# Performance work log

Measured on AMD Instinct MI355X. Metric: run time of the kernel, lower is better.

## Reference

```python
import jax, jax.numpy as jnp
import numpy as np

N = 4096      # nnode
F = 128       # feature_dim
E = 64        # embed_dim
P_EDGE = 0.01 # edge probability (~41 avg degree)
NEG = -9e15
ALPHA = 0.2   # leaky relu slope


def _xavier(key, shape):
    lim = float(np.sqrt(6.0 / (shape[0] + shape[1])))
    return jax.random.uniform(key, shape, minval=-lim, maxval=lim, dtype=jnp.float32)


def setup_inputs() -> dict:
    key = jax.random.key(0)
    ks = jax.random.split(key, 14)
    features = jax.random.normal(ks[0], (N, F), dtype=jnp.float32)
    eye = jnp.eye(N, dtype=jnp.float32)

    def make_adj(k):
        a = (jax.random.uniform(k, (N, N)) < P_EDGE).astype(jnp.float32)
        return jnp.maximum(a, eye)  # self loop so no empty rows

    return {
        "features": features,
        "geo_adj": make_adj(ks[1]),
        "forward_adj": make_adj(ks[2]),
        "backward_adj": make_adj(ks[3]),
        "weight": _xavier(ks[4], (E, F)),
        "Wf": _xavier(ks[5], (F, E)),
        "af1": jax.random.normal(ks[6], (E,), dtype=jnp.float32) * 0.1,
        "af2": jax.random.normal(ks[7], (E,), dtype=jnp.float32) * 0.1,
        "Wb": _xavier(ks[8], (F, E)),
        "ab1": jax.random.normal(ks[9], (E,), dtype=jnp.float32) * 0.1,
        "ab2": jax.random.normal(ks[10], (E,), dtype=jnp.float32) * 0.1,
        "Wg": _xavier(ks[11], (F, E)),
        "ag1": jax.random.normal(ks[12], (E,), dtype=jnp.float32) * 0.1,
        "ag2": jax.random.normal(ks[13], (E,), dtype=jnp.float32) * 0.1,
    }


def _mean_neighbors(adj, feat):
    # pre_weight: row-normalized neighbor averaging, (N,N) @ (N,F)
    deg = jnp.clip(jnp.sum(adj, axis=1, keepdims=True), 1.0, None)
    return (adj @ feat) / deg


def _attention(feat, mask_feat, adj, W, a1, a2):
    # GAT-style additive attention with masked softmax over neighbors
    h = feat @ W        # (N, E)
    hm = mask_feat @ W  # (N, E)
    e = jax.nn.leaky_relu((h @ a1)[:, None] + (hm @ a2)[None, :], negative_slope=ALPHA)  # (N, N)
    e = jnp.where(adj > 0, e, NEG)
    return jax.nn.softmax(e, axis=1)  # (N, N)


def reference(features, geo_adj, forward_adj, backward_adj, weight,
              Wf, af1, af2, Wb, ab1, ab2, Wg, ag1, ag2):
    t = features  # (N, F)
    mask_f = _mean_neighbors(forward_adj, t)
    mask_b = _mean_neighbors(backward_adj, t)
    mask_g = _mean_neighbors(geo_adj, t)

    w_f = _attention(t, mask_f, forward_adj, Wf, af1, af2)
    w_b = _attention(t, mask_b, backward_adj, Wb, ab1, ab2)
    w_g = _attention(t, mask_g, geo_adj, Wg, ag1, ag2)

    # get_mask_matrix_i/_j broadcast-mul + sum(1) == attn @ t (or attn.T @ t)
    x = weight @ t.T                  # (E, N)
    x_fwd = weight @ (w_f @ t).T      # mask_matrix_i
    x_bwd = weight @ (w_b.T @ t).T    # mask_matrix_j (transposed)
    x_geo = weight @ (w_g @ t).T      # mask_matrix_i

    return jnp.concatenate([x, x_fwd, x_bwd, x_geo], axis=0)  # (4E, N)
```

## Files before the change

### kernel.cpp

```cpp
#include <hip/hip_runtime.h>

#define NN 4096
#define FF 128
#define EE 64

typedef unsigned short u16;
typedef unsigned long long u64;
typedef float vf4 __attribute__((ext_vector_type(4)));

__device__ __forceinline__ float lrelu(float x) { return x > 0.f ? x : 0.2f * x; }

__global__ __launch_bounds__(256)
void k_pre(const float* __restrict__ t, const float* __restrict__ weight,
           const float* __restrict__ Wf, const float* __restrict__ af1, const float* __restrict__ af2,
           const float* __restrict__ Wb, const float* __restrict__ ab1, const float* __restrict__ ab2,
           const float* __restrict__ Wg, const float* __restrict__ ag1, const float* __restrict__ ag2,
           float* __restrict__ u, float* __restrict__ s1, float* __restrict__ p,
           float* __restrict__ out, int* __restrict__ ccnt)
{
    __shared__ float ww[64 * 129];
    __shared__ float tt[16 * 130];
    __shared__ float uacc[64 * 17];
    __shared__ float w6[6 * FF];
    int b = blockIdx.x, tid = threadIdx.x;

    if (b < 64) {
        if (b < 16) ccnt[b * 256 + tid] = 0;
        const float* Ws[3]  = {Wf, Wb, Wg};
        const float* a1s[3] = {af1, ab1, ag1};
        const float* a2s[3] = {af2, ab2, ag2};
        for (int idx = tid; idx < 768; idx += 256) {
            int vi = idx >> 7, f = idx & 127, dd = vi >> 1;
            const float4* a4 = reinterpret_cast<const float4*>((vi & 1) ? a2s[dd] : a1s[dd]);
            const float4* W4 = reinterpret_cast<const float4*>(Ws[dd] + (size_t)f * EE);
            float s = 0.f;
            #pragma unroll
            for (int e4 = 0; e4 < 16; ++e4) {
                float4 wv = W4[e4], av = a4[e4];
                s += wv.x * av.x + wv.y * av.y + wv.z * av.z + wv.w * av.w;
            }
            w6[vi * FF + f] = s;
        }
        __syncthreads();
        int nb = b * 64;
        for (int idx = tid; idx < 384; idx += 256) {
            int n = idx & 63, vi = idx >> 6;
            const float4* t4 = reinterpret_cast<const float4*>(t + (size_t)(nb + n) * FF);
            const float* wv = &w6[vi * FF];
            float s = 0.f;
            #pragma unroll 8
            for (int q4 = 0; q4 < 32; ++q4) {
                float4 v = t4[q4];
                s += v.x * wv[q4 * 4] + v.y * wv[q4 * 4 + 1]
                   + v.z * wv[q4 * 4 + 2] + v.w * wv[q4 * 4 + 3];
            }
            int dd = vi >> 1;
            if (vi & 1) p[dd * NN + nb + n] = s; else s1[dd * NN + nb + n] = s;
        }
        return;
    }

    int n0 = (b - 64) * 16;
    const float4* w4 = reinterpret_cast<const float4*>(weight);
    for (int i = tid; i < 2048; i += 256) {
        float4 v = w4[i];
        int fi = i * 4, e = fi >> 7, q = fi & 127;
        float* dst = &ww[e * 129 + q];
        dst[0] = v.x; dst[1] = v.y; dst[2] = v.z; dst[3] = v.w;
    }
    const float4* t4 = reinterpret_cast<const float4*>(t + (size_t)n0 * FF);
    for (int i = tid; i < 512; i += 256) {
        float4 v = t4[i];
        int fi = i * 4, nd = fi >> 7, q = fi & 127;
        float* dst = &tt[nd * 130 + q];
        dst[0] = v.x; dst[1] = v.y; dst[2] = v.z; dst[3] = v.w;
    }
    __syncthreads();
    int g = tid >> 6, lane = tid & 63;
    for (int k = 0; k < 4; ++k) {
        int nd = g * 4 + k;
        const float* trow = &tt[nd * 130];
        const float* wrow = &ww[lane * 129];
        float acc = 0.f;
        #pragma unroll 16
        for (int q = 0; q < 128; ++q) acc += wrow[q] * trow[q];
        u[(size_t)(n0 + nd) * EE + lane] = acc;
        uacc[lane * 17 + nd] = acc;
    }
    __syncthreads();
    int e = tid >> 2, io = (tid & 3) * 4;
    float* orow = out + (size_t)e * NN + n0 + io;
    orow[0] = uacc[e * 17 + io];
    orow[1] = uacc[e * 17 + io + 1];
    orow[2] = uacc[e * 17 + io + 2];
    orow[3] = uacc[e * 17 + io + 3];
}

__global__ __launch_bounds__(256, 8)
void k_scan(const float* __restrict__ Af, const float* __restrict__ Ab, const float* __restrict__ Ag,
            const float* __restrict__ p,
            u16* __restrict__ csr, int* __restrict__ cnt, float* __restrict__ s2,
            u16* __restrict__ csc, int* __restrict__ ccnt, int stride)
{
    int wid = threadIdx.x >> 6, lane = threadIdx.x & 63;
    int gw = blockIdx.x * 4 + wid;
    #pragma unroll 1
    for (int rr = 0; rr < 2; ++rr) {
        int gr = gw * 2 + rr;
        int d = gr >> 12, r = gr & (NN - 1);
        const float* A = d == 0 ? Af : (d == 1 ? Ab : Ag);
        const vf4* row4 = reinterpret_cast<const vf4*>(A + (size_t)r * NN);
        const float* pd = p + d * NN;

        u64 mask = 0ull;
        vf4 L[8];
        #pragma unroll
        for (int j = 0; j < 8; ++j) L[j] = __builtin_nontemporal_load(row4 + j * 64 + lane);
        #pragma unroll
        for (int j = 0; j < 8; ++j) {
            unsigned mm = (L[j].x != 0.f ? 1u : 0u) | (L[j].y != 0.f ? 2u : 0u) |
                          (L[j].z != 0.f ? 4u : 0u) | (L[j].w != 0.f ? 8u : 0u);
            mask |= ((u64)mm) << (j * 4);
        }
        #pragma unroll
        for (int j = 0; j < 8; ++j) L[j] = __builtin_nontemporal_load(row4 + (8 + j) * 64 + lane);
        #pragma unroll
        for (int j = 0; j < 8; ++j) {
            unsigned mm = (L[j].x != 0.f ? 1u : 0u) | (L[j].y != 0.f ? 2u : 0u) |
                          (L[j].z != 0.f ? 4u : 0u) | (L[j].w != 0.f ? 8u : 0u);
            mask |= ((u64)mm) << (32 + j * 4);
        }

        int lc = __popcll(mask);
        int sc = lc;
        for (int off = 1; off < 64; off <<= 1) {
            int o = __shfl_up(sc, off);
            if (lane >= off) sc += o;
        }
        int total = __shfl(sc, 63);
        int pos = sc - lc;
        u16* crow = csr + (size_t)gr * stride;
        float q = 0.f;
        u64 m = mask;
        while (m) {
            int bb = __ffsll(m) - 1;
            m &= m - 1;
            int col = ((bb >> 2) << 8) + (lane << 2) + (bb & 3);
            if (pos < stride) crow[pos] = (u16)col;
            pos++;
            q += pd[col];
            if (d == 1) {
                int cp = atomicAdd(&ccnt[col], 1);
                if (cp < stride) csc[(size_t)col * stride + cp] = (u16)r;
            }
        }
        for (int off = 32; off; off >>= 1) q += __shfl_xor(q, off);
        if (lane == 0) {
            cnt[gr] = total;
            s2[gr] = q / fmaxf((float)total, 1.f);
        }
    }
}

__global__ void k_zb(const float* __restrict__ s1, const float* __restrict__ s2,
                     const u16* __restrict__ csr, const int* __restrict__ cnt, int stride,
                     float* __restrict__ Zb)
{
    int tid = threadIdx.x, wave = tid >> 6, lane = tid & 63;
    int j = blockIdx.x * 4 + wave;
    int gr = NN + j;
    int nnz = min(cnt[gr], stride);
    const u16* crow = csr + (size_t)gr * stride;
    float s1j = s1[gr];
    const float* s2b = s2 + NN;
    float z = 0.f;
    if (lane < nnz)      z += __expf(lrelu(s1j + s2b[crow[lane]]));
    if (lane + 64 < nnz) z += __expf(lrelu(s1j + s2b[crow[lane + 64]]));
    for (int off = 32; off; off >>= 1) z += __shfl_xor(z, off);
    if (lane == 0) Zb[j] = z;
}

__global__ __launch_bounds__(256)
void k_out(const float* __restrict__ u,
           const float* __restrict__ s1, const float* __restrict__ s2,
           const float* __restrict__ Zb,
           const u16* __restrict__ csr, const int* __restrict__ cnt,
           const u16* __restrict__ csc, const int* __restrict__ ccnt, int stride,
           float* __restrict__ out)
{
    __shared__ float oacc[16 * 66];
    int gr0 = blockIdx.x * 16;
    int d = gr0 >> 12, i0 = gr0 & (NN - 1);
    int wid = threadIdx.x >> 6, lane = threadIdx.x & 63;
    for (int k = 0; k < 4; ++k) {
        int lr = k * 4 + wid;
        int i = i0 + lr;
        int gr = gr0 + lr;
        int nnz;
        int c0v = 0, c1v = 0;
        float w0v = 0.f, w1v = 0.f;
        if (d == 1) {
            nnz = min(ccnt[i], stride);
            const u16* cc = csc + (size_t)i * stride;
            float s2i = s2[NN + i];
            if (lane < nnz)      { int j = cc[lane];      c0v = j; w0v = __expf(lrelu(s1[NN + j] + s2i)) / Zb[j]; }
            if (lane + 64 < nnz) { int j = cc[lane + 64]; c1v = j; w1v = __expf(lrelu(s1[NN + j] + s2i)) / Zb[j]; }
        } else {
            nnz = min(cnt[gr], stride);
            const u16* crow = csr + (size_t)gr * stride;
            float s1i = s1[gr];
            const float* s2d = s2 + d * NN;
            float z = 0.f;
            if (lane < nnz)      { int c = crow[lane];      c0v = c; w0v = __expf(lrelu(s1i + s2d[c])); z += w0v; }
            if (lane + 64 < nnz) { int c = crow[lane + 64]; c1v = c; w1v = __expf(lrelu(s1i + s2d[c])); z += w1v; }
            for (int off = 32; off; off >>= 1) z += __shfl_xor(z, off);
            float invz = z > 0.f ? 1.f / z : 0.f;
            w0v *= invz; w1v *= invz;
        }
        float a0 = 0.f, a1 = 0.f, a2 = 0.f, a3 = 0.f;
        int n0c = nnz < 64 ? nnz : 64;
        int kk = 0;
        for (; kk + 3 < n0c; kk += 4) {
            int ca = __shfl(c0v, kk),     cb = __shfl(c0v, kk + 1);
            int cc2 = __shfl(c0v, kk + 2), cd = __shfl(c0v, kk + 3);
            float wa = __shfl(w0v, kk),     wb = __shfl(w0v, kk + 1);
            float wc = __shfl(w0v, kk + 2), wd = __shfl(w0v, kk + 3);
            a0 += wa * u[(size_t)ca  * EE + lane];
            a1 += wb * u[(size_t)cb  * EE + lane];
            a2 += wc * u[(size_t)cc2 * EE + lane];
            a3 += wd * u[(size_t)cd  * EE + lane];
        }
        for (; kk < n0c; ++kk)
            a0 += __shfl(w0v, kk) * u[(size_t)__shfl(c0v, kk) * EE + lane];
        int n1c = nnz - 64;
        kk = 0;
        for (; kk + 3 < n1c; kk += 4) {
            int ca = __shfl(c1v, kk),     cb = __shfl(c1v, kk + 1);
            int cc2 = __shfl(c1v, kk + 2), cd = __shfl(c1v, kk + 3);
            float wa = __shfl(w1v, kk),     wb = __shfl(w1v, kk + 1);
            float wc = __shfl(w1v, kk + 2), wd = __shfl(w1v, kk + 3);
            a0 += wa * u[(size_t)ca  * EE + lane];
            a1 += wb * u[(size_t)cb  * EE + lane];
            a2 += wc * u[(size_t)cc2 * EE + lane];
            a3 += wd * u[(size_t)cd  * EE + lane];
        }
        for (; kk < n1c; ++kk)
            a0 += __shfl(w1v, kk) * u[(size_t)__shfl(c1v, kk) * EE + lane];
        oacc[lr * 66 + lane] = (a0 + a1) + (a2 + a3);
    }
    __syncthreads();
    int e = threadIdx.x >> 2, io = (threadIdx.x & 3) * 4;
    int base = 64 + (d << 6);
    float* orow = out + (size_t)(base + e) * NN + i0 + io;
    orow[0] = oacc[(io    ) * 66 + e];
    orow[1] = oacc[(io + 1) * 66 + e];
    orow[2] = oacc[(io + 2) * 66 + e];
    orow[3] = oacc[(io + 3) * 66 + e];
}

extern "C" void kernel_launch(void* const* d_in, const int* in_sizes, int n_in,
                              void* d_out, int out_size, void* d_ws, size_t ws_size,
                              hipStream_t stream)
{
    const float* t   = (const float*)d_in[0];
    const float* Ag  = (const float*)d_in[1];
    const float* Af  = (const float*)d_in[2];
    const float* Ab  = (const float*)d_in[3];
    const float* W   = (const float*)d_in[4];
    const float* Wf  = (const float*)d_in[5];
    const float* af1 = (const float*)d_in[6];
    const float* af2 = (const float*)d_in[7];
    const float* Wb  = (const float*)d_in[8];
    const float* ab1 = (const float*)d_in[9];
    const float* ab2 = (const float*)d_in[10];
    const float* Wg  = (const float*)d_in[11];
    const float* ag1 = (const float*)d_in[12];
    const float* ag2 = (const float*)d_in[13];
    float* out = (float*)d_out;

    float* ws = (float*)d_ws;
    float* v6  = ws;
    float* s1  = v6 + 6 * FF;
    float* p   = s1 + 3 * NN;
    float* s2  = p + 3 * NN;
    float* Zb  = s2 + 3 * NN;
    float* u   = Zb + NN;
    int*   cnt  = (int*)(u + (size_t)NN * EE);
    int*   ccnt = cnt + 3 * NN;
    u16*   csr  = (u16*)(ccnt + NN);

    size_t base_bytes = ((char*)csr) - ((char*)d_ws);
    int stride = 128;
    if (base_bytes + (size_t)4 * NN * 128 * 2 > ws_size) stride = 96;
    if (base_bytes + (size_t)4 * NN * 96 * 2 > ws_size)  stride = 64;
    u16* csc = csr + (size_t)3 * NN * stride;

    k_pre<<<320, 256, 0, stream>>>(t, W, Wf, af1, af2, Wb, ab1, ab2, Wg, ag1, ag2,
                                   u, s1, p, out, ccnt);
    k_scan<<<1536, 256, 0, stream>>>(Af, Ab, Ag, p, csr, cnt, s2, csc, ccnt, stride);
    k_zb<<<NN / 4, 256, 0, stream>>>(s1, s2, csr, cnt, stride, Zb);
    k_out<<<3 * NN / 16, 256, 0, stream>>>(u, s1, s2, Zb, csr, cnt, csc, ccnt, stride, out);
}
```

Measured before the change: 245.7 us.

## Fuse four kernel launches into one cooperative persistent kernel with grid syncs

Replaces the four separate launches (pre, scan, zb, out) with a single cooperative kernel of 1536 blocks that separates the phases with grid.sync(), keeping the old launches as a fallback if the cooperative launch fails. The goal is to remove launch gaps and tail effects between phases. The pre phase is also re-tiled: 512 blocks of 8 nodes each compute u in two k-passes, and outputs are written as float2. The risks are that all 1536 blocks must be co-resident (256 MI355X CUs × 6 blocks), grid barriers have their own cost, and the scan phase now assigns rows gw and gw+6144 rather than consecutive pairs.

```diff
diff --git a/kernel.cpp b/kernel.cpp
--- a/kernel.cpp
+++ b/kernel.cpp
@@ -1,14 +1,258 @@
 #include <hip/hip_runtime.h>
+#include <hip/hip_cooperative_groups.h>
+
+namespace cg = cooperative_groups;
 
 #define NN 4096
 #define FF 128
 #define EE 64
+#define NBLK 1536
 
 typedef unsigned short u16;
 typedef unsigned long long u64;
 typedef float vf4 __attribute__((ext_vector_type(4)));
 
 __device__ __forceinline__ float lrelu(float x) { return x > 0.f ? x : 0.2f * x; }
+
+__global__ __launch_bounds__(256, 6)
+void k_all(const float* __restrict__ t, const float* __restrict__ weight,
+           const float* __restrict__ Af, const float* __restrict__ Ab, const float* __restrict__ Ag,
+           const float* __restrict__ Wf, const float* __restrict__ af1, const float* __restrict__ af2,
+           const float* __restrict__ Wb, const float* __restrict__ ab1, const float* __restrict__ ab2,
+           const float* __restrict__ Wg, const float* __restrict__ ag1, const float* __restrict__ ag2,
+           float* __restrict__ u, float* __restrict__ s1, float* __restrict__ p,
+           float* __restrict__ s2, float* __restrict__ Zb,
+           int* __restrict__ cnt, int* __restrict__ ccnt,
+           u16* __restrict__ csr, u16* __restrict__ csc, int stride,
+           float* __restrict__ out)
+{
+    __shared__ float smem[5776];
+    cg::grid_group grid = cg::this_grid();
+    int b = blockIdx.x, tid = threadIdx.x;
+    int wid = tid >> 6, lane = tid & 63;
+
+    if (b < 512) {
+        int n0 = b * 8;
+        float* ww   = smem;
+        float* tt   = smem + 4160;
+        float* uacc = smem + 5200;
+        {
+            const float4* t4 = reinterpret_cast<const float4*>(t + (size_t)n0 * FF);
+            float4 v = t4[tid];
+            int nd = tid >> 5, q = (tid & 31) * 4;
+            float* dst = &tt[nd * 129 + q];
+            dst[0] = v.x; dst[1] = v.y; dst[2] = v.z; dst[3] = v.w;
+        }
+        int ndA = wid * 2, ndB = wid * 2 + 1;
+        float accA = 0.f, accB = 0.f;
+        const float4* w4 = reinterpret_cast<const float4*>(weight);
+        for (int pass = 0; pass < 2; ++pass) {
+            __syncthreads();
+            for (int i = tid; i < 1024; i += 256) {
+                int e = i >> 4, kk4 = i & 15;
+                float4 v = w4[e * 32 + pass * 16 + kk4];
+                float* dst = &ww[e * 65 + kk4 * 4];
+                dst[0] = v.x; dst[1] = v.y; dst[2] = v.z; dst[3] = v.w;
+            }
+            __syncthreads();
+            const float* ta = &tt[ndA * 129 + pass * 64];
+            const float* tb = &tt[ndB * 129 + pass * 64];
+            const float* we = &ww[lane * 65];
+            #pragma unroll 16
+            for (int kk = 0; kk < 64; ++kk) {
+                float wv = we[kk];
+                accA += wv * ta[kk];
+                accB += wv * tb[kk];
+            }
+        }
+        u[(size_t)(n0 + ndA) * EE + lane] = accA;
+        u[(size_t)(n0 + ndB) * EE + lane] = accB;
+        uacc[lane * 9 + ndA] = accA;
+        uacc[lane * 9 + ndB] = accB;
+        __syncthreads();
+        int e = tid >> 2, np = tid & 3;
+        float2 v2 = make_float2(uacc[e * 9 + np * 2], uacc[e * 9 + np * 2 + 1]);
+        *reinterpret_cast<float2*>(out + (size_t)e * NN + n0 + np * 2) = v2;
+    } else if (b < 576) {
+        if (b < 528) ccnt[(b - 512) * 256 + tid] = 0;
+        float* w6 = smem;
+        const float* Ws[3]  = {Wf, Wb, Wg};
+        const float* a1s[3] = {af1, ab1, ag1};
+        const float* a2s[3] = {af2, ab2, ag2};
+        for (int idx = tid; idx < 768; idx += 256) {
+            int vi = idx >> 7, f = idx & 127, dd = vi >> 1;
+            const float4* a4 = reinterpret_cast<const float4*>((vi & 1) ? a2s[dd] : a1s[dd]);
+            const float4* W4 = reinterpret_cast<const float4*>(Ws[dd] + (size_t)f * EE);
+            float s = 0.f;
+            #pragma unroll
+            for (int e4 = 0; e4 < 16; ++e4) {
+                float4 wv = W4[e4], av = a4[e4];
+                s += wv.x * av.x + wv.y * av.y + wv.z * av.z + wv.w * av.w;
+            }
+            w6[vi * FF + f] = s;
+        }
+        __syncthreads();
+        int nb = (b - 512) * 64;
+        for (int idx = tid; idx < 384; idx += 256) {
+            int n = idx & 63, vi = idx >> 6;
+            const float4* t4 = reinterpret_cast<const float4*>(t + (size_t)(nb + n) * FF);
+            const float* wv = &w6[vi * FF];
+            float s = 0.f;
+            #pragma unroll 8
+            for (int q4 = 0; q4 < 32; ++q4) {
+                float4 v = t4[q4];
+                s += v.x * wv[q4 * 4] + v.y * wv[q4 * 4 + 1]
+                   + v.z * wv[q4 * 4 + 2] + v.w * wv[q4 * 4 + 3];
+            }
+            int dd = vi >> 1;
+            if (vi & 1) p[dd * NN + nb + n] = s; else s1[dd * NN + nb + n] = s;
+        }
+    }
+    grid.sync();
+
+    {
+        int gw = b * 4 + wid;
+        #pragma unroll 1
+        for (int rr = 0; rr < 2; ++rr) {
+            int gr = rr == 0 ? gw : gw + 6144;
+            int d = gr >> 12, r = gr & (NN - 1);
+            const float* A = d == 0 ? Af : (d == 1 ? Ab : Ag);
+            const vf4* row4 = reinterpret_cast<const vf4*>(A + (size_t)r * NN);
+            const float* pd = p + d * NN;
+
+            u64 mask = 0ull;
+            vf4 L[8];
+            #pragma unroll
+            for (int j = 0; j < 8; ++j) L[j] = __builtin_nontemporal_load(row4 + j * 64 + lane);
+            #pragma unroll
+            for (int j = 0; j < 8; ++j) {
+                unsigned mm = (L[j].x != 0.f ? 1u : 0u) | (L[j].y != 0.f ? 2u : 0u) |
+                              (L[j].z != 0.f ? 4u : 0u) | (L[j].w != 0.f ? 8u : 0u);
+                mask |= ((u64)mm) << (j * 4);
+            }
+            #pragma unroll
+            for (int j = 0; j < 8; ++j) L[j] = __builtin_nontemporal_load(row4 + (8 + j) * 64 + lane);
+            #pragma unroll
+            for (int j = 0; j < 8; ++j) {
+                unsigned mm = (L[j].x != 0.f ? 1u : 0u) | (L[j].y != 0.f ? 2u : 0u) |
+                              (L[j].z != 0.f ? 4u : 0u) | (L[j].w != 0.f ? 8u : 0u);
+                mask |= ((u64)mm) << (32 + j * 4);
+            }
+
+            int lc = __popcll(mask);
+            int sc = lc;
+            for (int off = 1; off < 64; off <<= 1) {
+                int o = __shfl_up(sc, off);
+                if (lane >= off) sc += o;
+            }
+            int total = __shfl(sc, 63);
+            int pos = sc - lc;
+            u16* crow = csr + (size_t)gr * stride;
+            float q = 0.f;
+            u64 m = mask;
+            while (m) {
+                int bb = __ffsll(m) - 1;
+                m &= m - 1;
+                int col = ((bb >> 2) << 8) + (lane << 2) + (bb & 3);
+                if (pos < stride) crow[pos] = (u16)col;
+                pos++;
+                q += pd[col];
+                if (d == 1) {
+                    int cp = atomicAdd(&ccnt[col], 1);
+                    if (cp < stride) csc[(size_t)col * stride + cp] = (u16)r;
+                }
+            }
+            for (int off = 32; off; off >>= 1) q += __shfl_xor(q, off);
+            if (lane == 0) {
+                cnt[gr] = total;
+                s2[gr] = q / fmaxf((float)total, 1.f);
+            }
+        }
+    }
+    grid.sync();
+
+    if (b < 1024) {
+        int j = b * 4 + wid;
+        int gr = NN + j;
+        int nnz = min(cnt[gr], stride);
+        const u16* crow = csr + (size_t)gr * stride;
+        float s1j = s1[gr];
+        const float* s2b = s2 + NN;
+        float z = 0.f;
+        if (lane < nnz)      z += __expf(lrelu(s1j + s2b[crow[lane]]));
+        if (lane + 64 < nnz) z += __expf(lrelu(s1j + s2b[crow[lane + 64]]));
+        for (int off = 32; off; off >>= 1) z += __shfl_xor(z, off);
+        if (lane == 0) Zb[j] = z;
+    }
+    grid.sync();
+
+    {
+        float* oacc = smem;
+        int gr0 = b * 8;
+        int d = gr0 >> 12, i0 = gr0 & (NN - 1);
+        for (int rr = 0; rr < 2; ++rr) {
+            int lr = wid * 2 + rr;
+            int i = i0 + lr;
+            int gr = gr0 + lr;
+            int nnz;
+            int c0v = 0, c1v = 0;
+            float w0v = 0.f, w1v = 0.f;
+            if (d == 1) {
+                nnz = min(ccnt[i], stride);
+                const u16* cc = csc + (size_t)i * stride;
+                float s2i = s2[NN + i];
+                if (lane < nnz)      { int j = cc[lane];      c0v = j; w0v = __expf(lrelu(s1[NN + j] + s2i)) / Zb[j]; }
+                if (lane + 64 < nnz) { int j = cc[lane + 64]; c1v = j; w1v = __expf(lrelu(s1[NN + j] + s2i)) / Zb[j]; }
+            } else {
+                nnz = min(cnt[gr], stride);
+                const u16* crow = csr + (size_t)gr * stride;
+                float s1i = s1[gr];
+                const float* s2d = s2 + d * NN;
+                float z = 0.f;
+                if (lane < nnz)      { int c = crow[lane];      c0v = c; w0v = __expf(lrelu(s1i + s2d[c])); z += w0v; }
+                if (lane + 64 < nnz) { int c = crow[lane + 64]; c1v = c; w1v = __expf(lrelu(s1i + s2d[c])); z += w1v; }
+                for (int off = 32; off; off >>= 1) z += __shfl_xor(z, off);
+                float invz = z > 0.f ? 1.f / z : 0.f;
+                w0v *= invz; w1v *= invz;
+            }
+            float a0 = 0.f, a1 = 0.f, a2 = 0.f, a3 = 0.f;
+            int n0c = nnz < 64 ? nnz : 64;
+            int kk = 0;
+            for (; kk + 3 < n0c; kk += 4) {
+                int ca = __shfl(c0v, kk),      cb = __shfl(c0v, kk + 1);
+                int cc2 = __shfl(c0v, kk + 2), cd = __shfl(c0v, kk + 3);
+                float wa = __shfl(w0v, kk),      wb = __shfl(w0v, kk + 1);
+                float wc = __shfl(w0v, kk + 2),  wd = __shfl(w0v, kk + 3);
+                a0 += wa * u[(size_t)ca  * EE + lane];
+                a1 += wb * u[(size_t)cb  * EE + lane];
+                a2 += wc * u[(size_t)cc2 * EE + lane];
+                a3 += wd * u[(size_t)cd  * EE + lane];
+            }
+            for (; kk < n0c; ++kk)
+                a0 += __shfl(w0v, kk) * u[(size_t)__shfl(c0v, kk) * EE + lane];
+            int n1c = nnz - 64;
+            kk = 0;
+            for (; kk + 3 < n1c; kk += 4) {
+                int ca = __shfl(c1v, kk),      cb = __shfl(c1v, kk + 1);
+                int cc2 = __shfl(c1v, kk + 2), cd = __shfl(c1v, kk + 3);
+                float wa = __shfl(w1v, kk),      wb = __shfl(w1v, kk + 1);
+                float wc = __shfl(w1v, kk + 2),  wd = __shfl(w1v, kk + 3);
+                a0 += wa * u[(size_t)ca  * EE + lane];
+                a1 += wb * u[(size_t)cb  * EE + lane];
+                a2 += wc * u[(size_t)cc2 * EE + lane];
+                a3 += wd * u[(size_t)cd  * EE + lane];
+            }
+            for (; kk < n1c; ++kk)
+                a0 += __shfl(w1v, kk) * u[(size_t)__shfl(c1v, kk) * EE + lane];
+            oacc[lr * 66 + lane] = (a0 + a1) + (a2 + a3);
+        }
+        __syncthreads();
+        int e = tid >> 2, np = tid & 3;
+        int base = 64 + (d << 6);
+        float2 v2 = make_float2(oacc[(np * 2) * 66 + e], oacc[(np * 2 + 1) * 66 + e]);
+        *reinterpret_cast<float2*>(out + (size_t)(base + e) * NN + i0 + np * 2) = v2;
+    }
+}
 
 __global__ __launch_bounds__(256)
 void k_pre(const float* __restrict__ t, const float* __restrict__ weight,
@@ -23,7 +267,6 @@
     __shared__ float uacc[64 * 17];
     __shared__ float w6[6 * FF];
     int b = blockIdx.x, tid = threadIdx.x;
-
     if (b < 64) {
         if (b < 16) ccnt[b * 256 + tid] = 0;
         const float* Ws[3]  = {Wf, Wb, Wg};
@@ -59,7 +302,6 @@
         }
         return;
     }
-
     int n0 = (b - 64) * 16;
     const float4* w4 = reinterpret_cast<const float4*>(weight);
     for (int i = tid; i < 2048; i += 256) {
@@ -111,7 +353,6 @@
         const float* A = d == 0 ? Af : (d == 1 ? Ab : Ag);
         const vf4* row4 = reinterpret_cast<const vf4*>(A + (size_t)r * NN);
         const float* pd = p + d * NN;
-
         u64 mask = 0ull;
         vf4 L[8];
         #pragma unroll
@@ -130,7 +371,6 @@
                           (L[j].z != 0.f ? 4u : 0u) | (L[j].w != 0.f ? 8u : 0u);
             mask |= ((u64)mm) << (32 + j * 4);
         }
-
         int lc = __popcll(mask);
         int sc = lc;
         for (int off = 1; off < 64; off <<= 1) {
@@ -221,10 +461,10 @@
         int n0c = nnz < 64 ? nnz : 64;
         int kk = 0;
         for (; kk + 3 < n0c; kk += 4) {
-            int ca = __shfl(c0v, kk),     cb = __shfl(c0v, kk + 1);
+            int ca = __shfl(c0v, kk),      cb = __shfl(c0v, kk + 1);
             int cc2 = __shfl(c0v, kk + 2), cd = __shfl(c0v, kk + 3);
-            float wa = __shfl(w0v, kk),     wb = __shfl(w0v, kk + 1);
-            float wc = __shfl(w0v, kk + 2), wd = __shfl(w0v, kk + 3);
+            float wa = __shfl(w0v, kk),      wb = __shfl(w0v, kk + 1);
+            float wc = __shfl(w0v, kk + 2),  wd = __shfl(w0v, kk + 3);
             a0 += wa * u[(size_t)ca  * EE + lane];
             a1 += wb * u[(size_t)cb  * EE + lane];
             a2 += wc * u[(size_t)cc2 * EE + lane];
@@ -235,10 +475,10 @@
         int n1c = nnz - 64;
         kk = 0;
         for (; kk + 3 < n1c; kk += 4) {
-            int ca = __shfl(c1v, kk),     cb = __shfl(c1v, kk + 1);
+            int ca = __shfl(c1v, kk),      cb = __shfl(c1v, kk + 1);
             int cc2 = __shfl(c1v, kk + 2), cd = __shfl(c1v, kk + 3);
-            float wa = __shfl(w1v, kk),     wb = __shfl(w1v, kk + 1);
-            float wc = __shfl(w1v, kk + 2), wd = __shfl(w1v, kk + 3);
+            float wa = __shfl(w1v, kk),      wb = __shfl(w1v, kk + 1);
+            float wc = __shfl(w1v, kk + 2),  wd = __shfl(w1v, kk + 3);
             a0 += wa * u[(size_t)ca  * EE + lane];
             a1 += wb * u[(size_t)cb  * EE + lane];
             a2 += wc * u[(size_t)cc2 * EE + lane];
@@ -295,9 +535,23 @@
     if (base_bytes + (size_t)4 * NN * 96 * 2 > ws_size)  stride = 64;
     u16* csc = csr + (size_t)3 * NN * stride;
 
-    k_pre<<<320, 256, 0, stream>>>(t, W, Wf, af1, af2, Wb, ab1, ab2, Wg, ag1, ag2,
-                                   u, s1, p, out, ccnt);
-    k_scan<<<1536, 256, 0, stream>>>(Af, Ab, Ag, p, csr, cnt, s2, csc, ccnt, stride);
-    k_zb<<<NN / 4, 256, 0, stream>>>(s1, s2, csr, cnt, stride, Zb);
-    k_out<<<3 * NN / 16, 256, 0, stream>>>(u, s1, s2, Zb, csr, cnt, csc, ccnt, stride, out);
+    void* args[] = {
+        (void*)&t, (void*)&W, (void*)&Af, (void*)&Ab, (void*)&Ag,
+        (void*)&Wf, (void*)&af1, (void*)&af2,
+        (void*)&Wb, (void*)&ab1, (void*)&ab2,
+        (void*)&Wg, (void*)&ag1, (void*)&ag2,
+        (void*)&u, (void*)&s1, (void*)&p, (void*)&s2, (void*)&Zb,
+        (void*)&cnt, (void*)&ccnt, (void*)&csr, (void*)&csc, (void*)&stride,
+        (void*)&out
+    };
+    hipError_t err = hipLaunchCooperativeKernel((const void*)k_all,
+                                                dim3(NBLK), dim3(256),
+                                                args, 0, stream);
+    if (err != hipSuccess) {
+        k_pre<<<320, 256, 0, stream>>>(t, W, Wf, af1, af2, Wb, ab1, ab2, Wg, ag1, ag2,
+                                       u, s1, p, out, ccnt);
+        k_scan<<<1536, 256, 0, stream>>>(Af, Ab, Ag, p, csr, cnt, s2, csc, ccnt, stride);
+        k_zb<<<NN / 4, 256, 0, stream>>>(s1, s2, csr, cnt, stride, Zb);
+        k_out<<<3 * NN / 16, 256, 0, stream>>>(u, s1, s2, Zb, csr, cnt, csc, ccnt, stride, out);
+    }
 }
```

New measurement: 773.1 us. 3.15x slower.
